# Kernel optimization log

Measured on AMD Instinct MI355X. Metric: run time of the kernel, lower is better.

The kernel has to match this reference:

```python
import jax, jax.numpy as jnp
import numpy as np

B, T, IN, H, STEPS = 32768, 11, 2, 64, 80


def gru_cell(x, h, W_ih, W_hh, b_ih, b_hh):
    # PyTorch GRU cell: gates ordered (r, z, n)
    gi = x @ W_ih.T + b_ih            # [B, 3H]
    gh = h @ W_hh.T + b_hh            # [B, 3H]
    gi_r, gi_z, gi_n = jnp.split(gi, 3, axis=-1)
    gh_r, gh_z, gh_n = jnp.split(gh, 3, axis=-1)
    r = jax.nn.sigmoid(gi_r + gh_r)
    z = jax.nn.sigmoid(gi_z + gh_z)
    n = jnp.tanh(gi_n + r * gh_n)
    return (1.0 - z) * n + z * h


def setup_inputs() -> dict:
    key = jax.random.key(0)
    ks = jax.random.split(key, 20)
    s = 1.0 / np.sqrt(H)
    u = lambda k, shape: jax.random.uniform(k, shape, jnp.float32, -s, s)
    inp = {"x": jax.random.normal(ks[0], (B, T, IN), jnp.float32)}
    i = 1
    for pfx, in0 in (("e", IN), ("d", IN)):
        for l, d_in in ((0, in0), (1, H)):
            inp[f"{pfx}W_ih{l}"] = u(ks[i], (3 * H, d_in)); i += 1
            inp[f"{pfx}W_hh{l}"] = u(ks[i], (3 * H, H)); i += 1
            inp[f"{pfx}b_ih{l}"] = u(ks[i], (3 * H,)); i += 1
            inp[f"{pfx}b_hh{l}"] = u(ks[i], (3 * H,)); i += 1
    inp["fc_W"] = u(ks[17], (2, H))
    inp["fc_b"] = u(ks[18], (2,))
    return inp


def reference(x, eW_ih0, eW_hh0, eb_ih0, eb_hh0, eW_ih1, eW_hh1, eb_ih1, eb_hh1,
              dW_ih0, dW_hh0, db_ih0, db_hh0, dW_ih1, dW_hh1, db_ih1, db_hh1,
              fc_W, fc_b):
    b = x.shape[0]
    h0 = jnp.zeros((b, H), x.dtype)
    h1 = jnp.zeros((b, H), x.dtype)

    # ---- encoder: 2-layer GRU over time (dropout inactive in eval) ----
    def enc_step(carry, xt):
        c0, c1 = carry
        c0 = gru_cell(xt, c0, eW_ih0, eW_hh0, eb_ih0, eb_hh0)
        c1 = gru_cell(c0, c1, eW_ih1, eW_hh1, eb_ih1, eb_hh1)
        return (c0, c1), None

    (h0, h1), _ = jax.lax.scan(enc_step, (h0, h1), jnp.swapaxes(x, 0, 1))

    def dec_step(carry, _):
        inp, c0, c1 = carry
        c0 = gru_cell(inp, c0, dW_ih0, dW_hh0, db_ih0, db_hh0)
        c1 = gru_cell(c0, c1, dW_ih1, dW_hh1, db_ih1, db_hh1)
        pred = c1 @ fc_W.T + fc_b     # [B, 2]
        return (pred, c0, c1), pred

    init = (x[:, -1, :], h0, h1)
    _, preds = jax.lax.scan(dec_step, init, None, length=STEPS)  # [80, B, 2]
    return jnp.swapaxes(preds, 0, 1)  # [B, 80, 2]
```

## Files before the change

kernel.cpp:

```cpp
#include <hip/hip_runtime.h>
#include <cstddef>

#define T_SEQ 11
#define STEPS 80
#define SRC (-1.44269504f)
#define SNC ( 2.88539008f)

typedef _Float16 f16;
typedef _Float16 f16x4 __attribute__((ext_vector_type(4)));
typedef _Float16 f16x8 __attribute__((ext_vector_type(8)));
typedef float    f32x4 __attribute__((ext_vector_type(4)));

#define W0H   0
#define W1H   12288
#define W1X   24576
#define W0X   36864
#define WPADO 49152
#define HB    55296
#define BIASH 71680
#define LDS_BYTES (71680*2 + 768*4)

__device__ __forceinline__ f32x4 mfma16(f16x8 a, f16x8 b, f32x4 c) {
    return __builtin_amdgcn_mfma_f32_16x16x32_f16(a, b, c, 0, 0, 0);
}

__device__ __forceinline__ void stage_w(f16* lds, int dst, const float* __restrict__ W, int tid) {
    for (int c = tid; c < 1536; c += 512) {
        const int row = c >> 3, kc = c & 7;
        const float sc = (row < 128) ? SRC : SNC;
        const float* p = W + row * 64 + kc * 8;
        f16x8 v;
        #pragma unroll
        for (int i = 0; i < 8; ++i) v[i] = (f16)(sc * p[i]);
        *(f16x8*)(lds + dst + row * 64 + ((kc ^ (row & 7)) << 3)) = v;
    }
}
__device__ __forceinline__ void stage_comp(f16* lds, int dst, const float* __restrict__ Wih0,
                                           const float* __restrict__ fcW, int tid) {
    for (int c = tid; c < 1536; c += 512) {
        const int row = c >> 3, kc = c & 7;
        const float sc = (row < 128) ? SRC : SNC;
        const float a = Wih0[row * 2], b = Wih0[row * 2 + 1];
        f16x8 v;
        #pragma unroll
        for (int i = 0; i < 8; ++i)
            v[i] = (f16)(sc * (a * fcW[kc * 8 + i] + b * fcW[64 + kc * 8 + i]));
        *(f16x8*)(lds + dst + row * 64 + ((kc ^ (row & 7)) << 3)) = v;
    }
}
__device__ __forceinline__ void stage_pad(f16* lds, const float* __restrict__ Wih0, int tid) {
    for (int c = tid; c < 768; c += 512) {
        const int row = c >> 2, kc = c & 3;
        const float sc = (row < 128) ? SRC : SNC;
        f16x8 v;
        #pragma unroll
        for (int i = 0; i < 8; ++i) v[i] = (f16)0.f;
        if (kc == 0) { v[0] = (f16)(sc * Wih0[row * 2]); v[1] = (f16)(sc * Wih0[row * 2 + 1]); }
        *(f16x8*)(lds + WPADO + row * 32 + ((kc ^ (row & 3)) << 3)) = v;
    }
}
__device__ __forceinline__ void stage_bias(float* bb, int base, const float* __restrict__ bih,
                                           const float* __restrict__ bhh, int tid) {
    for (int t = tid; t < 256; t += 512) {
        const int a = t >> 6, j = t & 63;
        float v;
        if (a == 0)      v = SRC * (bih[j] + bhh[j]);
        else if (a == 1) v = SRC * (bih[64 + j] + bhh[64 + j]);
        else if (a == 2) v = SNC * bih[128 + j];
        else             v = SNC * bhh[128 + j];
        bb[(base + a) * 64 + j] = v;
    }
}
__device__ __forceinline__ void stage_bias_fold(float* bb, int base, const float* __restrict__ bih,
    const float* __restrict__ bhh, const float* __restrict__ Wih0, const float* __restrict__ fcb, int tid) {
    const float f0 = fcb[0], f1 = fcb[1];
    for (int t = tid; t < 256; t += 512) {
        const int a = t >> 6, j = t & 63;
        float v;
        if (a == 0)      { const int r = j;       v = SRC * (bih[r] + bhh[r] + Wih0[r*2]*f0 + Wih0[r*2+1]*f1); }
        else if (a == 1) { const int r = 64 + j;  v = SRC * (bih[r] + bhh[r] + Wih0[r*2]*f0 + Wih0[r*2+1]*f1); }
        else if (a == 2) { const int r = 128 + j; v = SNC * (bih[r] + Wih0[r*2]*f0 + Wih0[r*2+1]*f1); }
        else             v = SNC * bhh[128 + j];
        bb[(base + a) * 64 + j] = v;
    }
}

struct Lane {
    int col, quad, c7, colr, x0, x1;
    int wo[4];
};

template<bool PADX>
__device__ __forceinline__ void cell_(f16* lds, int awh, int awx, int hxoff, int hhoff,
                                      int barr, const Lane& L, f16x4 (&ho)[4], f16x8 xpb)
{
    const float* bb = (const float*)(lds + BIASH);
    f16x8 xb0, xb1;
    if constexpr (!PADX) {
        xb0 = *(const f16x8*)(lds + hxoff + L.colr + L.x0);
        xb1 = *(const f16x8*)(lds + hxoff + L.colr + L.x1);
    }
    f16x8 hb0 = *(const f16x8*)(lds + hhoff + L.colr + L.x0);
    f16x8 hb1 = *(const f16x8*)(lds + hhoff + L.colr + L.x1);
    #pragma unroll
    for (int mtj = 0; mtj < 4; ++mtj) {
        const int bj = mtj * 16 + L.quad * 4;
        f32x4 bR  = *(const f32x4*)(bb + (barr + 0) * 64 + bj);
        f32x4 bZ  = *(const f32x4*)(bb + (barr + 1) * 64 + bj);
        f32x4 bNi = *(const f32x4*)(bb + (barr + 2) * 64 + bj);
        f32x4 bNh = *(const f32x4*)(bb + (barr + 3) * 64 + bj);
        const int ar = (mtj * 16 + L.col) * 64;
        f16x8 hR0 = *(const f16x8*)(lds + awh        + ar + L.x0);
        f16x8 hR1 = *(const f16x8*)(lds + awh        + ar + L.x1);
        f16x8 hZ0 = *(const f16x8*)(lds + awh + 4096 + ar + L.x0);
        f16x8 hZ1 = *(const f16x8*)(lds + awh + 4096 + ar + L.x1);
        f16x8 hN0 = *(const f16x8*)(lds + awh + 8192 + ar + L.x0);
        f16x8 hN1 = *(const f16x8*)(lds + awh + 8192 + ar + L.x1);
        f32x4 aR  = mfma16(hR0, hb0, bR);  aR  = mfma16(hR1, hb1, aR);
        f32x4 aZ  = mfma16(hZ0, hb0, bZ);  aZ  = mfma16(hZ1, hb1, aZ);
        f32x4 aNh = mfma16(hN0, hb0, bNh); aNh = mfma16(hN1, hb1, aNh);
        f32x4 aNi;
        if constexpr (PADX) {
            const int xp = (L.quad ^ (L.col & 3)) << 3;
            const int pr = (mtj * 16 + L.col) * 32;
            f16x8 pR = *(const f16x8*)(lds + WPADO        + pr + xp);
            f16x8 pZ = *(const f16x8*)(lds + WPADO + 2048 + pr + xp);
            f16x8 pN = *(const f16x8*)(lds + WPADO + 4096 + pr + xp);
            aR  = mfma16(pR, xpb, aR);
            aZ  = mfma16(pZ, xpb, aZ);
            aNi = mfma16(pN, xpb, bNi);
        } else {
            f16x8 xR0 = *(const f16x8*)(lds + awx        + ar + L.x0);
            f16x8 xR1 = *(const f16x8*)(lds + awx        + ar + L.x1);
            f16x8 xZ0 = *(const f16x8*)(lds + awx + 4096 + ar + L.x0);
            f16x8 xZ1 = *(const f16x8*)(lds + awx + 4096 + ar + L.x1);
            f16x8 xN0 = *(const f16x8*)(lds + awx + 8192 + ar + L.x0);
            f16x8 xN1 = *(const f16x8*)(lds + awx + 8192 + ar + L.x1);
            aR  = mfma16(xR0, xb0, aR);   aR  = mfma16(xR1, xb1, aR);
            aZ  = mfma16(xZ0, xb0, aZ);   aZ  = mfma16(xZ1, xb1, aZ);
            aNi = mfma16(xN0, xb0, bNi);  aNi = mfma16(xN1, xb1, aNi);
        }
        f16x4 o;
        #pragma unroll
        for (int i = 0; i < 4; ++i) {
            const float r = __builtin_amdgcn_rcpf(1.f + __builtin_amdgcn_exp2f(aR[i]));
            const float z = __builtin_amdgcn_rcpf(1.f + __builtin_amdgcn_exp2f(aZ[i]));
            const float n = 1.f - 2.f * __builtin_amdgcn_rcpf(1.f + __builtin_amdgcn_exp2f(aNi[i] + r * aNh[i]));
            const float h = n + z * ((float)ho[mtj][i] - n);
            o[i] = (f16)h;
        }
        ho[mtj] = o;
        *(f16x4*)(lds + hhoff + L.wo[mtj]) = o;
    }
}

__global__ __launch_bounds__(512, 2)
void gru_wave(
    const float* __restrict__ x,
    const float* __restrict__ eWih0, const float* __restrict__ eWhh0,
    const float* __restrict__ ebih0, const float* __restrict__ ebhh0,
    const float* __restrict__ eWih1, const float* __restrict__ eWhh1,
    const float* __restrict__ ebih1, const float* __restrict__ ebhh1,
    const float* __restrict__ dWih0, const float* __restrict__ dWhh0,
    const float* __restrict__ dbih0, const float* __restrict__ dbhh0,
    const float* __restrict__ dWih1, const float* __restrict__ dWhh1,
    const float* __restrict__ dbih1, const float* __restrict__ dbhh1,
    const float* __restrict__ fcW,  const float* __restrict__ fcb,
    float* __restrict__ out)
{
    extern __shared__ f16 lds[];
    float* bb = (float*)(lds + BIASH);
    const int tid  = threadIdx.x;
    const int lane = tid & 63;
    const int wv   = __builtin_amdgcn_readfirstlane(tid >> 6);

    Lane L;
    L.col  = lane & 15;
    L.quad = lane >> 4;
    L.c7   = L.col & 7;
    L.colr = L.col * 64;
    L.x0   = (L.quad ^ L.c7) << 3;
    L.x1   = ((4 + L.quad) ^ L.c7) << 3;
    #pragma unroll
    for (int mtj = 0; mtj < 4; ++mtj)
        L.wo[mtj] = L.colr + (((2 * mtj + (L.quad >> 1)) ^ L.c7) << 3) + ((L.quad & 1) << 2);

    const int r0    = blockIdx.x * 128;
    const int myrow = r0 + wv * 16 + L.col;
    const int h0off = HB + wv * 2048;
    const int h1off = h0off + 1024;

    stage_w(lds, W0H, eWhh0, tid);
    stage_w(lds, W1H, eWhh1, tid);
    stage_w(lds, W1X, eWih1, tid);
    stage_pad(lds, eWih0, tid);
    stage_bias(bb, 0, ebih0, ebhh0, tid);
    stage_bias(bb, 4, ebih1, ebhh1, tid);
    {
        f16x8 z;
        #pragma unroll
        for (int i = 0; i < 8; ++i) z[i] = (f16)0.f;
        for (int k = lane; k < 256; k += 64) *(f16x8*)(lds + h0off + k * 8) = z;
    }
    f16x4 ho0[4], ho1[4];
    #pragma unroll
    for (int m = 0; m < 4; ++m) {
        #pragma unroll
        for (int i = 0; i < 4; ++i) { ho0[m][i] = (f16)0.f; ho1[m][i] = (f16)0.f; }
    }
    __syncthreads();

    const float* xrow = x + (size_t)myrow * (T_SEQ * 2);
    f16x8 zf;
    #pragma unroll
    for (int i = 0; i < 8; ++i) zf[i] = (f16)0.f;

    #pragma unroll 1
    for (int t = 0; t < T_SEQ; ++t) {
        const float2 xv = *(const float2*)(xrow + t * 2);
        f16x8 xpb = zf;
        if (L.quad == 0) { xpb[0] = (f16)xv.x; xpb[1] = (f16)xv.y; }
        cell_<true >(lds, W0H, 0,   0,     h0off, 0, L, ho0, xpb);
        cell_<false>(lds, W1H, W1X, h0off, h1off, 4, L, ho1, zf);
    }

    __syncthreads();
    stage_w(lds, W0H, dWhh0, tid);
    stage_w(lds, W1H, dWhh1, tid);
    stage_w(lds, W1X, dWih1, tid);
    stage_comp(lds, W0X, dWih0, fcW, tid);
    stage_pad(lds, dWih0, tid);
    stage_bias_fold(bb, 0, dbih0, dbhh0, dWih0, fcb, tid);
    stage_bias(bb, 4, dbih1, dbhh1, tid);
    stage_bias(bb, 8, dbih0, dbhh0, tid);
    __syncthreads();

    f16x8 fcf0 = zf, fcf1 = zf;
    if (L.col < 2) {
        #pragma unroll
        for (int i = 0; i < 8; ++i) {
            fcf0[i] = (f16)fcW[L.col * 64 + L.quad * 8 + i];
            fcf1[i] = (f16)fcW[L.col * 64 + 32 + L.quad * 8 + i];
        }
    }
    f32x4 pb;
    #pragma unroll
    for (int rg = 0; rg < 4; ++rg) pb[rg] = (L.quad == 0 && rg < 2) ? fcb[rg] : 0.f;

    float* __restrict__ outp = out + (size_t)myrow * (STEPS * 2);

    {
        const float2 xv = *(const float2*)(xrow + (T_SEQ - 1) * 2);
        f16x8 xpb = zf;
        if (L.quad == 0) { xpb[0] = (f16)xv.x; xpb[1] = (f16)xv.y; }
        cell_<true >(lds, W0H, 0,   0,     h0off, 8, L, ho0, xpb);
        cell_<false>(lds, W1H, W1X, h0off, h1off, 4, L, ho1, zf);
        f16x8 b0 = *(const f16x8*)(lds + h1off + L.colr + L.x0);
        f16x8 b1 = *(const f16x8*)(lds + h1off + L.colr + L.x1);
        f32x4 p = mfma16(fcf0, b0, pb);
        p = mfma16(fcf1, b1, p);
        if (L.quad == 0) *(float2*)outp = make_float2(p[0], p[1]);
    }

    #pragma unroll 1
    for (int s = 1; s < STEPS; ++s) {
        cell_<false>(lds, W0H, W0X, h1off, h0off, 0, L, ho0, zf);
        cell_<false>(lds, W1H, W1X, h0off, h1off, 4, L, ho1, zf);
        f16x8 b0 = *(const f16x8*)(lds + h1off + L.colr + L.x0);
        f16x8 b1 = *(const f16x8*)(lds + h1off + L.colr + L.x1);
        f32x4 p = mfma16(fcf0, b0, pb);
        p = mfma16(fcf1, b1, p);
        if (L.quad == 0) *(float2*)(outp + s * 2) = make_float2(p[0], p[1]);
    }
}

extern "C" void kernel_launch(void* const* d_in, const int* in_sizes, int n_in,
                              void* d_out, int out_size, void* d_ws, size_t ws_size,
                              hipStream_t stream) {
    (void)n_in; (void)out_size; (void)d_ws; (void)ws_size;

    const float* x     = (const float*)d_in[0];
    const float* eWih0 = (const float*)d_in[1];
    const float* eWhh0 = (const float*)d_in[2];
    const float* ebih0 = (const float*)d_in[3];
    const float* ebhh0 = (const float*)d_in[4];
    const float* eWih1 = (const float*)d_in[5];
    const float* eWhh1 = (const float*)d_in[6];
    const float* ebih1 = (const float*)d_in[7];
    const float* ebhh1 = (const float*)d_in[8];
    const float* dWih0 = (const float*)d_in[9];
    const float* dWhh0 = (const float*)d_in[10];
    const float* dbih0 = (const float*)d_in[11];
    const float* dbhh0 = (const float*)d_in[12];
    const float* dWih1 = (const float*)d_in[13];
    const float* dWhh1 = (const float*)d_in[14];
    const float* dbih1 = (const float*)d_in[15];
    const float* dbhh1 = (const float*)d_in[16];
    const float* fcW   = (const float*)d_in[17];
    const float* fcb   = (const float*)d_in[18];
    float* out = (float*)d_out;

    static int attr_set = hipFuncSetAttribute((const void*)gru_wave,
        hipFuncAttributeMaxDynamicSharedMemorySize, LDS_BYTES);
    (void)attr_set;
    hipFuncSetAttribute((const void*)gru_wave,
        hipFuncAttributeMaxDynamicSharedMemorySize, LDS_BYTES);

    const int b = in_sizes[0] / (T_SEQ * 2);
    dim3 grid(b / 128), block(512);
    hipLaunchKernelGGL(gru_wave, grid, block, LDS_BYTES, stream,
        x, eWih0, eWhh0, ebih0, ebhh0, eWih1, eWhh1, ebih1, ebhh1,
        dWih0, dWhh0, dbih0, dbhh0, dWih1, dWhh1, dbih1, dbhh1,
        fcW, fcb, out);
}
```

Before: 509.2 us.

## Hold layer-1 recurrent weights in registers and drop folded fc input path

```diff
diff --git a/kernel.cpp b/kernel.cpp
--- a/kernel.cpp
+++ b/kernel.cpp
@@ -12,13 +12,11 @@
 typedef float    f32x4 __attribute__((ext_vector_type(4)));
 
 #define W0H   0
-#define W1H   12288
-#define W1X   24576
-#define W0X   36864
-#define WPADO 49152
-#define HB    55296
-#define BIASH 71680
-#define LDS_BYTES (71680*2 + 768*4)
+#define W1X   12288
+#define WPADO 24576
+#define HB    30720
+#define BIASH 47104
+#define LDS_BYTES (47104*2 + 512*4)
 
 __device__ __forceinline__ f32x4 mfma16(f16x8 a, f16x8 b, f32x4 c) {
     return __builtin_amdgcn_mfma_f32_16x16x32_f16(a, b, c, 0, 0, 0);
@@ -32,19 +30,6 @@
         f16x8 v;
         #pragma unroll
         for (int i = 0; i < 8; ++i) v[i] = (f16)(sc * p[i]);
-        *(f16x8*)(lds + dst + row * 64 + ((kc ^ (row & 7)) << 3)) = v;
-    }
-}
-__device__ __forceinline__ void stage_comp(f16* lds, int dst, const float* __restrict__ Wih0,
-                                           const float* __restrict__ fcW, int tid) {
-    for (int c = tid; c < 1536; c += 512) {
-        const int row = c >> 3, kc = c & 7;
-        const float sc = (row < 128) ? SRC : SNC;
-        const float a = Wih0[row * 2], b = Wih0[row * 2 + 1];
-        f16x8 v;
-        #pragma unroll
-        for (int i = 0; i < 8; ++i)
-            v[i] = (f16)(sc * (a * fcW[kc * 8 + i] + b * fcW[64 + kc * 8 + i]));
         *(f16x8*)(lds + dst + row * 64 + ((kc ^ (row & 7)) << 3)) = v;
     }
 }
@@ -71,91 +56,124 @@
         bb[(base + a) * 64 + j] = v;
     }
 }
-__device__ __forceinline__ void stage_bias_fold(float* bb, int base, const float* __restrict__ bih,
-    const float* __restrict__ bhh, const float* __restrict__ Wih0, const float* __restrict__ fcb, int tid) {
-    const float f0 = fcb[0], f1 = fcb[1];
-    for (int t = tid; t < 256; t += 512) {
-        const int a = t >> 6, j = t & 63;
-        float v;
-        if (a == 0)      { const int r = j;       v = SRC * (bih[r] + bhh[r] + Wih0[r*2]*f0 + Wih0[r*2+1]*f1); }
-        else if (a == 1) { const int r = 64 + j;  v = SRC * (bih[r] + bhh[r] + Wih0[r*2]*f0 + Wih0[r*2+1]*f1); }
-        else if (a == 2) { const int r = 128 + j; v = SNC * (bih[r] + Wih0[r*2]*f0 + Wih0[r*2+1]*f1); }
-        else             v = SNC * bhh[128 + j];
-        bb[(base + a) * 64 + j] = v;
+
+__device__ __forceinline__ f16x8 wfrag(const float* __restrict__ W, int row, int k0, float sc) {
+    f16x8 r;
+    #pragma unroll
+    for (int i = 0; i < 8; ++i) r[i] = (f16)(sc * W[row * 64 + k0 + i]);
+    return r;
+}
+__device__ __forceinline__ void load_wregs(f16x8 (&R)[8], f16x8 (&Z)[8], f16x8 (&N)[8],
+                                           const float* __restrict__ Whh, int col, int quad) {
+    #pragma unroll
+    for (int ks = 0; ks < 2; ++ks) {
+        #pragma unroll
+        for (int mt = 0; mt < 4; ++mt) {
+            const int k0 = ks * 32 + quad * 8;
+            R[ks * 4 + mt] = wfrag(Whh, mt * 16 + col,       k0, SRC);
+            Z[ks * 4 + mt] = wfrag(Whh, 64  + mt * 16 + col, k0, SRC);
+            N[ks * 4 + mt] = wfrag(Whh, 128 + mt * 16 + col, k0, SNC);
+        }
     }
 }
 
 struct Lane {
-    int col, quad, c7, colr, x0, x1;
+    int col, quad, c7, colr, x0, x1, xp;
     int wo[4];
 };
 
-template<bool PADX>
-__device__ __forceinline__ void cell_(f16* lds, int awh, int awx, int hxoff, int hhoff,
-                                      int barr, const Lane& L, f16x4 (&ho)[4], f16x8 xpb)
+__device__ __forceinline__ void cell_l0(f16* lds, const Lane& L, f16x4 (&ho)[4],
+                                        f16x8 xpb, int h0off)
 {
     const float* bb = (const float*)(lds + BIASH);
-    f16x8 xb0, xb1;
-    if constexpr (!PADX) {
-        xb0 = *(const f16x8*)(lds + hxoff + L.colr + L.x0);
-        xb1 = *(const f16x8*)(lds + hxoff + L.colr + L.x1);
-    }
-    f16x8 hb0 = *(const f16x8*)(lds + hhoff + L.colr + L.x0);
-    f16x8 hb1 = *(const f16x8*)(lds + hhoff + L.colr + L.x1);
-    #pragma unroll
-    for (int mtj = 0; mtj < 4; ++mtj) {
-        const int bj = mtj * 16 + L.quad * 4;
-        f32x4 bR  = *(const f32x4*)(bb + (barr + 0) * 64 + bj);
-        f32x4 bZ  = *(const f32x4*)(bb + (barr + 1) * 64 + bj);
-        f32x4 bNi = *(const f32x4*)(bb + (barr + 2) * 64 + bj);
-        f32x4 bNh = *(const f32x4*)(bb + (barr + 3) * 64 + bj);
-        const int ar = (mtj * 16 + L.col) * 64;
-        f16x8 hR0 = *(const f16x8*)(lds + awh        + ar + L.x0);
-        f16x8 hR1 = *(const f16x8*)(lds + awh        + ar + L.x1);
-        f16x8 hZ0 = *(const f16x8*)(lds + awh + 4096 + ar + L.x0);
-        f16x8 hZ1 = *(const f16x8*)(lds + awh + 4096 + ar + L.x1);
-        f16x8 hN0 = *(const f16x8*)(lds + awh + 8192 + ar + L.x0);
-        f16x8 hN1 = *(const f16x8*)(lds + awh + 8192 + ar + L.x1);
+    f16x8 hb0 = *(const f16x8*)(lds + h0off + L.colr + L.x0);
+    f16x8 hb1 = *(const f16x8*)(lds + h0off + L.colr + L.x1);
+    #pragma unroll
+    for (int mt = 0; mt < 4; ++mt) {
+        const int bj = mt * 16 + L.quad * 4;
+        f32x4 bR  = *(const f32x4*)(bb + 0 * 64 + bj);
+        f32x4 bZ  = *(const f32x4*)(bb + 1 * 64 + bj);
+        f32x4 bNi = *(const f32x4*)(bb + 2 * 64 + bj);
+        f32x4 bNh = *(const f32x4*)(bb + 3 * 64 + bj);
+        const int ar = (mt * 16 + L.col) * 64;
+        f16x8 hR0 = *(const f16x8*)(lds + W0H        + ar + L.x0);
+        f16x8 hR1 = *(const f16x8*)(lds + W0H        + ar + L.x1);
+        f16x8 hZ0 = *(const f16x8*)(lds + W0H + 4096 + ar + L.x0);
+        f16x8 hZ1 = *(const f16x8*)(lds + W0H + 4096 + ar + L.x1);
+        f16x8 hN0 = *(const f16x8*)(lds + W0H + 8192 + ar + L.x0);
+        f16x8 hN1 = *(const f16x8*)(lds + W0H + 8192 + ar + L.x1);
+        const int pr = (mt * 16 + L.col) * 32;
+        f16x8 pR = *(const f16x8*)(lds + WPADO        + pr + L.xp);
+        f16x8 pZ = *(const f16x8*)(lds + WPADO + 2048 + pr + L.xp);
+        f16x8 pN = *(const f16x8*)(lds + WPADO + 4096 + pr + L.xp);
         f32x4 aR  = mfma16(hR0, hb0, bR);  aR  = mfma16(hR1, hb1, aR);
         f32x4 aZ  = mfma16(hZ0, hb0, bZ);  aZ  = mfma16(hZ1, hb1, aZ);
         f32x4 aNh = mfma16(hN0, hb0, bNh); aNh = mfma16(hN1, hb1, aNh);
-        f32x4 aNi;
-        if constexpr (PADX) {
-            const int xp = (L.quad ^ (L.col & 3)) << 3;
-            const int pr = (mtj * 16 + L.col) * 32;
-            f16x8 pR = *(const f16x8*)(lds + WPADO        + pr + xp);
-            f16x8 pZ = *(const f16x8*)(lds + WPADO + 2048 + pr + xp);
-            f16x8 pN = *(const f16x8*)(lds + WPADO + 4096 + pr + xp);
-            aR  = mfma16(pR, xpb, aR);
-            aZ  = mfma16(pZ, xpb, aZ);
-            aNi = mfma16(pN, xpb, bNi);
-        } else {
-            f16x8 xR0 = *(const f16x8*)(lds + awx        + ar + L.x0);
-            f16x8 xR1 = *(const f16x8*)(lds + awx        + ar + L.x1);
-            f16x8 xZ0 = *(const f16x8*)(lds + awx + 4096 + ar + L.x0);
-            f16x8 xZ1 = *(const f16x8*)(lds + awx + 4096 + ar + L.x1);
-            f16x8 xN0 = *(const f16x8*)(lds + awx + 8192 + ar + L.x0);
-            f16x8 xN1 = *(const f16x8*)(lds + awx + 8192 + ar + L.x1);
-            aR  = mfma16(xR0, xb0, aR);   aR  = mfma16(xR1, xb1, aR);
-            aZ  = mfma16(xZ0, xb0, aZ);   aZ  = mfma16(xZ1, xb1, aZ);
-            aNi = mfma16(xN0, xb0, bNi);  aNi = mfma16(xN1, xb1, aNi);
-        }
+        aR  = mfma16(pR, xpb, aR);
+        aZ  = mfma16(pZ, xpb, aZ);
+        f32x4 aNi = mfma16(pN, xpb, bNi);
         f16x4 o;
         #pragma unroll
         for (int i = 0; i < 4; ++i) {
             const float r = __builtin_amdgcn_rcpf(1.f + __builtin_amdgcn_exp2f(aR[i]));
             const float z = __builtin_amdgcn_rcpf(1.f + __builtin_amdgcn_exp2f(aZ[i]));
             const float n = 1.f - 2.f * __builtin_amdgcn_rcpf(1.f + __builtin_amdgcn_exp2f(aNi[i] + r * aNh[i]));
-            const float h = n + z * ((float)ho[mtj][i] - n);
+            const float h = n + z * ((float)ho[mt][i] - n);
             o[i] = (f16)h;
         }
-        ho[mtj] = o;
-        *(f16x4*)(lds + hhoff + L.wo[mtj]) = o;
-    }
-}
-
-__global__ __launch_bounds__(512, 2)
-void gru_wave(
+        ho[mt] = o;
+        *(f16x4*)(lds + h0off + L.wo[mt]) = o;
+    }
+}
+
+__device__ __forceinline__ void cell_l1(f16* lds, const Lane& L, f16x4 (&ho)[4],
+    const f16x8 (&cR)[8], const f16x8 (&cZ)[8], const f16x8 (&cN)[8],
+    int h0off, int h1off)
+{
+    const float* bb = (const float*)(lds + BIASH);
+    f16x8 xb0 = *(const f16x8*)(lds + h0off + L.colr + L.x0);
+    f16x8 xb1 = *(const f16x8*)(lds + h0off + L.colr + L.x1);
+    f16x8 hb0 = *(const f16x8*)(lds + h1off + L.colr + L.x0);
+    f16x8 hb1 = *(const f16x8*)(lds + h1off + L.colr + L.x1);
+    #pragma unroll
+    for (int mt = 0; mt < 4; ++mt) {
+        const int bj = mt * 16 + L.quad * 4;
+        f32x4 bR  = *(const f32x4*)(bb + 4 * 64 + bj);
+        f32x4 bZ  = *(const f32x4*)(bb + 5 * 64 + bj);
+        f32x4 bNi = *(const f32x4*)(bb + 6 * 64 + bj);
+        f32x4 bNh = *(const f32x4*)(bb + 7 * 64 + bj);
+        const int ar = (mt * 16 + L.col) * 64;
+        f16x8 xR0 = *(const f16x8*)(lds + W1X        + ar + L.x0);
+        f16x8 xR1 = *(const f16x8*)(lds + W1X        + ar + L.x1);
+        f16x8 xZ0 = *(const f16x8*)(lds + W1X + 4096 + ar + L.x0);
+        f16x8 xZ1 = *(const f16x8*)(lds + W1X + 4096 + ar + L.x1);
+        f16x8 xN0 = *(const f16x8*)(lds + W1X + 8192 + ar + L.x0);
+        f16x8 xN1 = *(const f16x8*)(lds + W1X + 8192 + ar + L.x1);
+        f32x4 aR  = mfma16(cR[mt],     hb0, bR);
+        f32x4 aZ  = mfma16(cZ[mt],     hb0, bZ);
+        f32x4 aNh = mfma16(cN[mt],     hb0, bNh);
+        aR  = mfma16(cR[4 + mt], hb1, aR);
+        aZ  = mfma16(cZ[4 + mt], hb1, aZ);
+        aNh = mfma16(cN[4 + mt], hb1, aNh);
+        aR  = mfma16(xR0, xb0, aR);   aR  = mfma16(xR1, xb1, aR);
+        aZ  = mfma16(xZ0, xb0, aZ);   aZ  = mfma16(xZ1, xb1, aZ);
+        f32x4 aNi = mfma16(xN0, xb0, bNi); aNi = mfma16(xN1, xb1, aNi);
+        f16x4 o;
+        #pragma unroll
+        for (int i = 0; i < 4; ++i) {
+            const float r = __builtin_amdgcn_rcpf(1.f + __builtin_amdgcn_exp2f(aR[i]));
+            const float z = __builtin_amdgcn_rcpf(1.f + __builtin_amdgcn_exp2f(aZ[i]));
+            const float n = 1.f - 2.f * __builtin_amdgcn_rcpf(1.f + __builtin_amdgcn_exp2f(aNi[i] + r * aNh[i]));
+            const float h = n + z * ((float)ho[mt][i] - n);
+            o[i] = (f16)h;
+        }
+        ho[mt] = o;
+        *(f16x4*)(lds + h1off + L.wo[mt]) = o;
+    }
+}
+
+__global__ __launch_bounds__(512, 1)
+void gru_wave3(
     const float* __restrict__ x,
     const float* __restrict__ eWih0, const float* __restrict__ eWhh0,
     const float* __restrict__ ebih0, const float* __restrict__ ebhh0,
@@ -181,9 +199,10 @@
     L.colr = L.col * 64;
     L.x0   = (L.quad ^ L.c7) << 3;
     L.x1   = ((4 + L.quad) ^ L.c7) << 3;
-    #pragma unroll
-    for (int mtj = 0; mtj < 4; ++mtj)
-        L.wo[mtj] = L.colr + (((2 * mtj + (L.quad >> 1)) ^ L.c7) << 3) + ((L.quad & 1) << 2);
+    L.xp   = (L.quad ^ (L.col & 3)) << 3;
+    #pragma unroll
+    for (int mt = 0; mt < 4; ++mt)
+        L.wo[mt] = L.colr + (((2 * mt + (L.quad >> 1)) ^ L.c7) << 3) + ((L.quad & 1) << 2);
 
     const int r0    = blockIdx.x * 128;
     const int myrow = r0 + wv * 16 + L.col;
@@ -191,7 +210,6 @@
     const int h1off = h0off + 1024;
 
     stage_w(lds, W0H, eWhh0, tid);
-    stage_w(lds, W1H, eWhh1, tid);
     stage_w(lds, W1X, eWih1, tid);
     stage_pad(lds, eWih0, tid);
     stage_bias(bb, 0, ebih0, ebhh0, tid);
@@ -202,6 +220,8 @@
         for (int i = 0; i < 8; ++i) z[i] = (f16)0.f;
         for (int k = lane; k < 256; k += 64) *(f16x8*)(lds + h0off + k * 8) = z;
     }
+    f16x8 w1R[8], w1Z[8], w1N[8];
+    load_wregs(w1R, w1Z, w1N, eWhh1, L.col, L.quad);
     f16x4 ho0[4], ho1[4];
     #pragma unroll
     for (int m = 0; m < 4; ++m) {
@@ -220,19 +240,17 @@
         const float2 xv = *(const float2*)(xrow + t * 2);
         f16x8 xpb = zf;
         if (L.quad == 0) { xpb[0] = (f16)xv.x; xpb[1] = (f16)xv.y; }
-        cell_<true >(lds, W0H, 0,   0,     h0off, 0, L, ho0, xpb);
-        cell_<false>(lds, W1H, W1X, h0off, h1off, 4, L, ho1, zf);
+        cell_l0(lds, L, ho0, xpb, h0off);
+        cell_l1(lds, L, ho1, w1R, w1Z, w1N, h0off, h1off);
     }
 
     __syncthreads();
     stage_w(lds, W0H, dWhh0, tid);
-    stage_w(lds, W1H, dWhh1, tid);
     stage_w(lds, W1X, dWih1, tid);
-    stage_comp(lds, W0X, dWih0, fcW, tid);
     stage_pad(lds, dWih0, tid);
-    stage_bias_fold(bb, 0, dbih0, dbhh0, dWih0, fcb, tid);
+    stage_bias(bb, 0, dbih0, dbhh0, tid);
     stage_bias(bb, 4, dbih1, dbhh1, tid);
-    stage_bias(bb, 8, dbih0, dbhh0, tid);
+    load_wregs(w1R, w1Z, w1N, dWhh1, L.col, L.quad);
     __syncthreads();
 
     f16x8 fcf0 = zf, fcf1 = zf;
@@ -249,28 +267,26 @@
 
     float* __restrict__ outp = out + (size_t)myrow * (STEPS * 2);
 
+    f16x8 xpb = zf;
     {
         const float2 xv = *(const float2*)(xrow + (T_SEQ - 1) * 2);
-        f16x8 xpb = zf;
         if (L.quad == 0) { xpb[0] = (f16)xv.x; xpb[1] = (f16)xv.y; }
-        cell_<true >(lds, W0H, 0,   0,     h0off, 8, L, ho0, xpb);
-        cell_<false>(lds, W1H, W1X, h0off, h1off, 4, L, ho1, zf);
+    }
+
+    #pragma unroll 1
+    for (int s = 0; s < STEPS; ++s) {
+        cell_l0(lds, L, ho0, xpb, h0off);
+        cell_l1(lds, L, ho1, w1R, w1Z, w1N, h0off, h1off);
         f16x8 b0 = *(const f16x8*)(lds + h1off + L.colr + L.x0);
         f16x8 b1 = *(const f16x8*)(lds + h1off + L.colr + L.x1);
         f32x4 p = mfma16(fcf0, b0, pb);
         p = mfma16(fcf1, b1, p);
-        if (L.quad == 0) *(float2*)outp = make_float2(p[0], p[1]);
-    }
-
-    #pragma unroll 1
-    for (int s = 1; s < STEPS; ++s) {
-        cell_<false>(lds, W0H, W0X, h1off, h0off, 0, L, ho0, zf);
-        cell_<false>(lds, W1H, W1X, h0off, h1off, 4, L, ho1, zf);
-        f16x8 b0 = *(const f16x8*)(lds + h1off + L.colr + L.x0);
-        f16x8 b1 = *(const f16x8*)(lds + h1off + L.colr + L.x1);
-        f32x4 p = mfma16(fcf0, b0, pb);
-        p = mfma16(fcf1, b1, p);
-        if (L.quad == 0) *(float2*)(outp + s * 2) = make_float2(p[0], p[1]);
+        xpb = zf;
+        if (L.quad == 0) {
+            *(float2*)(outp + s * 2) = make_float2(p[0], p[1]);
+            xpb[0] = (f16)p[0];
+            xpb[1] = (f16)p[1];
+        }
     }
 }
 
@@ -300,15 +316,12 @@
     const float* fcb   = (const float*)d_in[18];
     float* out = (float*)d_out;
 
-    static int attr_set = hipFuncSetAttribute((const void*)gru_wave,
-        hipFuncAttributeMaxDynamicSharedMemorySize, LDS_BYTES);
-    (void)attr_set;
-    hipFuncSetAttribute((const void*)gru_wave,
+    hipFuncSetAttribute((const void*)gru_wave3,
         hipFuncAttributeMaxDynamicSharedMemorySize, LDS_BYTES);
 
     const int b = in_sizes[0] / (T_SEQ * 2);
     dim3 grid(b / 128), block(512);
-    hipLaunchKernelGGL(gru_wave, grid, block, LDS_BYTES, stream,
+    hipLaunchKernelGGL(gru_wave3, grid, block, LDS_BYTES, stream,
         x, eWih0, eWhh0, ebih0, ebhh0, eWih1, eWhh1, ebih1, ebhh1,
         dWih0, dWhh0, dbih0, dbhh0, dWih1, dWhh1, dbih1, dbhh1,
         fcW, fcb, out);
```

After: 480.9 us. -5.6%, faster.
